# Optimization experiments

Hardware: AMD Instinct MI355X
Metric: run time of the kernel (lower is better)

## Reference

```python
import jax, jax.numpy as jnp
import numpy as np
import math

B, S, D, H, FF = 2, 2048, 1024, 16, 4096
DH = D // H
EPS = 1e-5


def layernorm(x, g, b):
    mu = jnp.mean(x, axis=-1, keepdims=True)
    var = jnp.mean((x - mu) ** 2, axis=-1, keepdims=True)
    return (x - mu) * jax.lax.rsqrt(var + EPS) * g + b


def setup_inputs() -> dict:
    key = jax.random.key(0)
    ks = jax.random.split(key, 8)
    s = lambda fan_in: 1.0 / math.sqrt(fan_in)
    return {
        "x": jax.random.normal(ks[0], (B, S, D), jnp.float32),
        "attention_mask": jnp.zeros((B, 1, 1, S), jnp.float32),
        "wq": jax.random.uniform(ks[1], (D, D), jnp.float32, -s(D), s(D)),
        "wk": jax.random.uniform(ks[2], (D, D), jnp.float32, -s(D), s(D)),
        "wv": jax.random.uniform(ks[3], (D, D), jnp.float32, -s(D), s(D)),
        "wo": jax.random.uniform(ks[4], (D, D), jnp.float32, -s(D), s(D)),
        "w1": jax.random.uniform(ks[5], (D, FF), jnp.float32, -s(D), s(D)),
        "w2": jax.random.uniform(ks[6], (FF, D), jnp.float32, -s(FF), s(FF)),
        "ln1_g": jnp.ones((D,), jnp.float32),
        "ln1_b": jnp.zeros((D,), jnp.float32),
        "ln2_g": jnp.ones((D,), jnp.float32),
        "ln2_b": jnp.zeros((D,), jnp.float32),
    }


def reference(x, attention_mask, wq, wk, wv, wo, w1, w2, ln1_g, ln1_b, ln2_g, ln2_b):
    # --- attention ResNorm (pre-LN) ---
    y = layernorm(x, ln1_g, ln1_b)
    q = (y @ wq).reshape(B, S, H, DH)
    k = (y @ wk).reshape(B, S, H, DH)
    v = (y @ wv).reshape(B, S, H, DH)
    # NOTE: original scales by sqrt(hidden_dim), not sqrt(head_dim)
    scores = jnp.einsum("bqhd,bkhd->bhqk", q, k) / math.sqrt(D) + attention_mask
    probs = jax.nn.softmax(scores, axis=-1)
    attn = jnp.einsum("bhqk,bkhd->bqhd", probs, v).reshape(B, S, D)
    x = x + attn @ wo
    # --- FFN ResNorm ---
    y = layernorm(x, ln2_g, ln2_b)
    y = jax.nn.gelu(y @ w1, approximate=False) @ w2
    return x + y
```

## Files before the change

### kernel.cpp

```cpp
#include <hip/hip_runtime.h>
#include <hip/hip_bf16.h>
#include <math.h>

#define Bb 2
#define Ss 2048
#define Dd 1024
#define Hh 16
#define FFf 4096
#define EPSf 1e-5f
#define SCALEf 0.03125f
#define LOG2Ef 1.4426950408889634f
#define SCALE2f (SCALEf * LOG2Ef)
#define KSPLIT 2
#define NTILES ((Ss / KSPLIT) / 64)

typedef short s16x8 __attribute__((ext_vector_type(8)));
typedef short s16x4 __attribute__((ext_vector_type(4)));
typedef float f32x4 __attribute__((ext_vector_type(4)));
typedef float f32x16 __attribute__((ext_vector_type(16)));

__device__ __forceinline__ short f2bs(float f) {
    union { float f; unsigned u; } v; v.f = f;
    const unsigned r = (v.u + 0x7FFFu + ((v.u >> 16) & 1u)) >> 16;
    return (short)r;
}
__device__ __forceinline__ float bs2f(short s) {
    union { unsigned u; float f; } v; v.u = ((unsigned)(unsigned short)s) << 16;
    return v.f;
}
__device__ __forceinline__ float gelu_exact(float v) {
    return 0.5f * v * (1.0f + erff(v * 0.7071067811865475f));
}
__device__ __forceinline__ void gload16(const void* g, void* l) {
    __builtin_amdgcn_global_load_lds(
        (const __attribute__((address_space(1))) unsigned int*)g,
        (__attribute__((address_space(3))) unsigned int*)l, 16, 0, 0);
}
__device__ __forceinline__ unsigned cvt_pk(float lo, float hi) {
    unsigned r;
    asm("v_cvt_pk_bf16_f32 %0, %1, %2" : "=v"(r) : "v"(lo), "v"(hi));
    return r;
}

__global__ __launch_bounds__(256) void prep(const float* __restrict__ wq, const float* __restrict__ wk,
                                            const float* __restrict__ wv, const float* __restrict__ wo,
                                            const float* __restrict__ w1, const float* __restrict__ w2,
                                            const float* __restrict__ mask,
                                            short* __restrict__ qkvw_t, short* __restrict__ wot,
                                            short* __restrict__ w1t, short* __restrict__ w2t,
                                            float* __restrict__ msc) {
    const int blk = blockIdx.x;
    const int tid = threadIdx.x;
    if (blk >= 3072) {
#pragma unroll
        for (int j = 0; j < 16; ++j) msc[tid + j * 256] = mask[tid + j * 256] * LOG2Ef;
        return;
    }
    const float* W; short* Wt; int K, N, inner;
    if (blk < 1024) {
        const int which = blk >> 8; inner = blk & 255;
        K = 1024; N = 1024;
        W = (which == 0) ? wq : (which == 1) ? wk : (which == 2) ? wv : wo;
        Wt = (which < 3) ? qkvw_t + (size_t)which * 1024 * 1024 : wot;
    } else if (blk < 2048) {
        inner = blk - 1024; K = 1024; N = 4096; W = w1; Wt = w1t;
    } else {
        inner = blk - 2048; K = 4096; N = 1024; W = w2; Wt = w2t;
    }
    const int nbx = N / 64;
    const int bx = inner % nbx, by = inner / nbx;
    __shared__ short T[64][65];
    const int n0 = bx * 64, k0 = by * 64;
    const int c = tid & 63, rg = tid >> 6;
#pragma unroll
    for (int j = 0; j < 16; ++j) {
        const int r = rg * 16 + j;
        T[r][c] = f2bs(W[(size_t)(k0 + r) * N + n0 + c]);
    }
    __syncthreads();
#pragma unroll
    for (int j = 0; j < 16; ++j) {
        const int r = rg * 16 + j;
        Wt[(size_t)(n0 + r) * K + k0 + c] = T[c][r];
    }
}

__global__ __launch_bounds__(256) void vtranspose(const short* __restrict__ QKV,
                                                  short* __restrict__ VT) {
    __shared__ __align__(16) short T[64 * 144];
    const int t = threadIdx.x;
    const int bh = blockIdx.x;
    const int sc = blockIdx.y;
    const int b = bh >> 4, h = bh & 15;
#pragma unroll
    for (int i = 0; i < 4; ++i) {
        const int sl = i * 32 + (t >> 3);
        const int d0 = (t & 7) * 8;
        const s16x8 v = *(const s16x8*)&QKV[((size_t)(b * Ss + sc * 128 + sl)) * 3072 + 2048 + h * 64 + d0];
#pragma unroll
        for (int e = 0; e < 8; ++e) {
            const int d = d0 + e;
            T[(d * 144 + sl) ^ (((d >> 3) & 7) << 3)] = v[e];
        }
    }
    __syncthreads();
#pragma unroll
    for (int i = 0; i < 4; ++i) {
        const int d = i * 16 + (t >> 4);
        const int s0 = (t & 15) * 8;
        const s16x8 o = *(const s16x8*)&T[(d * 144 + s0) ^ (((d >> 3) & 7) << 3)];
        *(s16x8*)&VT[((size_t)(bh * 64 + d)) * 2048 + sc * 128 + s0] = o;
    }
}

__global__ __launch_bounds__(256) void layernorm_bf16(const float* __restrict__ X,
                                                      const float* __restrict__ g,
                                                      const float* __restrict__ bta,
                                                      short* __restrict__ Y) {
    __shared__ float red[8];
    const int row = blockIdx.x;
    const int tid = threadIdx.x;
    const size_t base = (size_t)row * Dd + tid * 4;
    const float4 xv = *(const float4*)&X[base];
    float s  = xv.x + xv.y + xv.z + xv.w;
    float sq = xv.x * xv.x + xv.y * xv.y + xv.z * xv.z + xv.w * xv.w;
#pragma unroll
    for (int o = 32; o >= 1; o >>= 1) {
        s  += __shfl_xor(s, o, 64);
        sq += __shfl_xor(sq, o, 64);
    }
    const int lane = tid & 63, wv = tid >> 6;
    if (lane == 0) { red[wv] = s; red[4 + wv] = sq; }
    __syncthreads();
    const float tot  = red[0] + red[1] + red[2] + red[3];
    const float totq = red[4] + red[5] + red[6] + red[7];
    const float mu  = tot * (1.0f / Dd);
    const float var = totq * (1.0f / Dd) - mu * mu;
    const float inv = 1.0f / sqrtf(var + EPSf);
    const float4 gv = *(const float4*)&g[tid * 4];
    const float4 bv = *(const float4*)&bta[tid * 4];
    s16x4 o;
    o[0] = f2bs((xv.x - mu) * inv * gv.x + bv.x);
    o[1] = f2bs((xv.y - mu) * inv * gv.y + bv.y);
    o[2] = f2bs((xv.z - mu) * inv * gv.z + bv.z);
    o[3] = f2bs((xv.w - mu) * inv * gv.w + bv.w);
    *(s16x4*)&Y[base] = o;
}

template <int EPI>
__global__ __launch_bounds__(256) void gemm_m97(const short* __restrict__ A,
                                                const short* __restrict__ Bt,
                                                void* __restrict__ Cout,
                                                int M, int N, int K, int gx) {
    __shared__ short As[128 * 32];
    __shared__ short Bs[128 * 32];
    const int tid = threadIdx.x;
    const int w = tid >> 6, l = tid & 63;
    const int lr = l & 15, lg = l >> 4;
    const int wr = w >> 1, wc = w & 1;

    const int nwg = gridDim.x;
    const int bid = blockIdx.x;
    const int swz = (bid & 7) * (nwg >> 3) + (bid >> 3);
    const int bx = swz % gx, by = swz / gx;

    const int srow = l >> 2;
    const int skb  = (l & 3) * 8;
    const size_t arow0 = (size_t)(by * 128 + w * 32);
    const size_t brow0 = (size_t)(bx * 128 + w * 32);

    f32x4 acc[4][4] = {};

    for (int k0 = 0; k0 < K; k0 += 32) {
        __syncthreads();
#pragma unroll
        for (int j = 0; j < 2; ++j) {
            gload16(A + (arow0 + j * 16 + srow) * K + k0 + skb,
                    &As[(w * 32 + j * 16) * 32]);
            gload16(Bt + (brow0 + j * 16 + srow) * K + k0 + skb,
                    &Bs[(w * 32 + j * 16) * 32]);
        }
        __syncthreads();
        s16x8 a[4], b[4];
#pragma unroll
        for (int m = 0; m < 4; ++m)
            a[m] = *(const s16x8*)&As[(wr * 64 + m * 16 + lr) * 32 + lg * 8];
#pragma unroll
        for (int n = 0; n < 4; ++n)
            b[n] = *(const s16x8*)&Bs[(wc * 64 + n * 16 + lr) * 32 + lg * 8];
#pragma unroll
        for (int n = 0; n < 4; ++n)
#pragma unroll
            for (int m = 0; m < 4; ++m)
                acc[n][m] = __builtin_amdgcn_mfma_f32_16x16x32_bf16(b[n], a[m], acc[n][m], 0, 0, 0);
    }

    const int row0 = by * 128 + wr * 64;
    const int col0 = bx * 128 + wc * 64;
#pragma unroll
    for (int m = 0; m < 4; ++m) {
        const int row = row0 + m * 16 + lr;
#pragma unroll
        for (int n = 0; n < 4; ++n) {
            const int cb = col0 + n * 16 + lg * 4;
            s16x4 o;
#pragma unroll
            for (int r = 0; r < 4; ++r) {
                float v = acc[n][m][r];
                if (EPI == 1) v = gelu_exact(v);
                o[r] = f2bs(v);
            }
            *(s16x4*)&((short*)Cout)[(size_t)row * N + cb] = o;
        }
    }
}

template <int BM, int BN, int BK, int EPI, int MW>
__global__ __launch_bounds__(256, MW) void gemm_v4(const short* __restrict__ A,
                                                   const short* __restrict__ Bt,
                                                   const float* __restrict__ R,
                                                   void* __restrict__ Cout,
                                                   int M, int N, int K, int gx) {
    constexpr int WM = BM / 2, WN = BN / 2;
    constexpr int MF = WM / 16, NF = WN / 16;
    constexpr int S   = BK / 8;
    constexpr int LPR = BK / 8;
    constexpr int RPI = 64 / LPR;
    constexpr int IPWA = (BM / 4) / RPI;
    constexpr int IPWB = (BN / 4) / RPI;
    __shared__ __align__(16) short As[2][BM * BK];
    __shared__ __align__(16) short Bs[2][BN * BK];

    const int tid = threadIdx.x;
    const int w = tid >> 6, l = tid & 63;
    const int lr = l & 15, lg = l >> 4;
    const int wr = w >> 1, wc = w & 1;

    const int nwg = gridDim.x;
    const int bid = blockIdx.x;
    const int swz = (bid & 7) * (nwg >> 3) + (bid >> 3);
    const int bx = swz % gx, by = swz / gx;

    const int lrow = l / LPR;
    const int sslot = ((l % LPR) ^ (((lrow * BK) >> 6) & (S - 1))) * 8;
    const size_t arow0 = (size_t)(by * BM);
    const size_t brow0 = (size_t)(bx * BN);

    f32x4 acc[NF][MF] = {};

    auto STAGE = [&](int bi, int k0) {
#pragma unroll
        for (int j = 0; j < IPWA; ++j) {
            const int r0 = w * (BM / 4) + j * RPI;
            gload16(A + (arow0 + r0 + lrow) * K + k0 + sslot, &As[bi][r0 * BK]);
        }
#pragma unroll
        for (int j = 0; j < IPWB; ++j) {
            const int r0 = w * (BN / 4) + j * RPI;
            gload16(Bt + (brow0 + r0 + lrow) * K + k0 + sslot, &Bs[bi][r0 * BK]);
        }
    };

    int aidx[BK / 32][MF], bidx[BK / 32][NF];
#pragma unroll
    for (int kk = 0; kk < BK / 32; ++kk) {
#pragma unroll
        for (int m = 0; m < MF; ++m) {
            const int r = wr * WM + m * 16 + lr;
            aidx[kk][m] = r * BK + ((kk * 4 + lg) ^ (((r * BK) >> 6) & (S - 1))) * 8;
        }
#pragma unroll
        for (int n = 0; n < NF; ++n) {
            const int r = wc * WN + n * 16 + lr;
            bidx[kk][n] = r * BK + ((kk * 4 + lg) ^ (((r * BK) >> 6) & (S - 1))) * 8;
        }
    }

    const int NKi = K / BK;
    STAGE(0, 0);

#pragma unroll 2
    for (int ks = 0; ks < NKi; ++ks) {
        const int cur = ks & 1;
        asm volatile("s_waitcnt vmcnt(0)" ::: "memory");
        __builtin_amdgcn_s_barrier();
        if (ks + 1 < NKi) STAGE(cur ^ 1, (ks + 1) * BK);

#pragma unroll
        for (int kk = 0; kk < BK / 32; ++kk) {
            s16x8 a[MF], b[NF];
#pragma unroll
            for (int m = 0; m < MF; ++m) a[m] = *(const s16x8*)&As[cur][aidx[kk][m]];
#pragma unroll
            for (int n = 0; n < NF; ++n) b[n] = *(const s16x8*)&Bs[cur][bidx[kk][n]];
#pragma unroll
            for (int n = 0; n < NF; ++n)
#pragma unroll
                for (int m = 0; m < MF; ++m)
                    acc[n][m] = __builtin_amdgcn_mfma_f32_16x16x32_bf16(b[n], a[m], acc[n][m], 0, 0, 0);
        }
    }

    const int row0 = by * BM + wr * WM;
    const int col0 = bx * BN + wc * WN;
#pragma unroll
    for (int m = 0; m < MF; ++m) {
        const int row = row0 + m * 16 + lr;
#pragma unroll
        for (int n = 0; n < NF; ++n) {
            const int cb = col0 + n * 16 + lg * 4;
            if (EPI == 2) {
                float* C = (float*)Cout;
                const f32x4 r4 = *(const f32x4*)&R[(size_t)row * N + cb];
                f32x4 o;
#pragma unroll
                for (int r = 0; r < 4; ++r) o[r] = acc[n][m][r] + r4[r];
                *(f32x4*)&C[(size_t)row * N + cb] = o;
            } else {
                s16x4 o;
#pragma unroll
                for (int r = 0; r < 4; ++r) {
                    float v = acc[n][m][r];
                    if (EPI == 1) v = gelu_exact(v);
                    o[r] = f2bs(v);
                }
                *(s16x4*)&((short*)Cout)[(size_t)row * N + cb] = o;
            }
        }
    }
}

__global__ __launch_bounds__(256, 4) void attn_split(const short* __restrict__ QKV,
                                                     const short* __restrict__ VT,
                                                     const float* __restrict__ MSC,
                                                     short* __restrict__ Opart,
                                                     float2* __restrict__ ML) {
    __shared__ __align__(16) short Kbuf[2][64 * 64];
    __shared__ __align__(16) short Vbuf[2][64 * 64];

    const int tid = threadIdx.x;
    const int w = tid >> 6, l = tid & 63;
    const int col = l & 31;
    const int hi = l >> 5;

    const int bid0 = blockIdx.x;
    const int bid = (bid0 & 7) * (gridDim.x >> 3) + (bid0 >> 3);
    const int part = bid >> 9;
    const int inner = bid & 511;
    const int qt = inner & 15, h = (inner >> 4) & 15, b = inner >> 8;
    const int q0 = qt * 128 + w * 32;
    const int k_base = part * (Ss / KSPLIT);

    s16x8 qf[4];
    {
        const short* qsrc = QKV + ((size_t)(b * Ss + q0 + col)) * 3072 + h * 64 + hi * 8;
        qf[0] = *(const s16x8*)(qsrc);
        qf[1] = *(const s16x8*)(qsrc + 16);
        qf[2] = *(const s16x8*)(qsrc + 32);
        qf[3] = *(const s16x8*)(qsrc + 48);
    }

    const int sr   = l >> 3;
    const int slot = ((l & 7) ^ (sr & 7)) * 8;
    const short* kg = QKV + (size_t)(b * Ss) * 3072 + 1024 + h * 64 + (size_t)sr * 3072 + slot;
    const short* vg = VT + ((size_t)(b * Hh + h) * 64 + sr) * 2048 + k_base + slot;
    const float* mscb = MSC + (size_t)b * Ss + k_base;

    int kidx[2][4], vidx[2][2][2];
#pragma unroll
    for (int sub = 0; sub < 2; ++sub) {
        const int rk = sub * 32 + col;
#pragma unroll
        for (int dd = 0; dd < 4; ++dd)
            kidx[sub][dd] = rk * 64 + ((2 * dd + hi) ^ (rk & 7)) * 8;
#pragma unroll
        for (int kk = 0; kk < 2; ++kk)
#pragma unroll
            for (int dt = 0; dt < 2; ++dt) {
                const int rv = dt * 32 + col;
                vidx[sub][kk][dt] = rv * 64 + ((sub * 4 + 2 * kk + hi) ^ (rv & 7)) * 8;
            }
    }

    f32x16 o_acc[2] = {};
    float m_used = -1e30f, l_run = 0.0f;

    auto STAGE = [&](int bi, int t) {
#pragma unroll
        for (int j = 0; j < 2; ++j) {
            const int r0 = w * 16 + j * 8;
            gload16(kg + (size_t)(k_base + t * 64 + r0) * 3072, &Kbuf[bi][r0 * 64]);
            gload16(vg + (size_t)r0 * 2048 + t * 64,             &Vbuf[bi][r0 * 64]);
        }
    };

    STAGE(0, 0);

#pragma unroll 2
    for (int i = 0; i < NTILES; ++i) {
        const int cur = i & 1;
        asm volatile("s_waitcnt vmcnt(0)" ::: "memory");
        __builtin_amdgcn_s_barrier();
        if (i + 1 < NTILES) STAGE(cur ^ 1, i + 1);

#pragma unroll
        for (int sub = 0; sub < 2; ++sub) {
            f32x16 sa = {};
#pragma unroll
            for (int dd = 0; dd < 4; ++dd) {
                const s16x8 kf = *(const s16x8*)&Kbuf[cur][kidx[sub][dd]];
                sa = __builtin_amdgcn_mfma_f32_32x32x16_bf16(kf, qf[dd], sa, 0, 0, 0);
            }

#pragma unroll
            for (int c4 = 0; c4 < 4; ++c4) {
                const f32x4 mv = *(const f32x4*)&mscb[i * 64 + sub * 32 + 8 * c4 + 4 * hi];
#pragma unroll
                for (int rr = 0; rr < 4; ++rr) sa[c4 * 4 + rr] = sa[c4 * 4 + rr] * SCALE2f + mv[rr];
            }
            float t8[8], t4[4];
#pragma unroll
            for (int r = 0; r < 8; ++r) t8[r] = fmaxf(sa[2 * r], sa[2 * r + 1]);
#pragma unroll
            for (int r = 0; r < 4; ++r) t4[r] = fmaxf(t8[2 * r], t8[2 * r + 1]);
            float tmax = fmaxf(fmaxf(t4[0], t4[1]), fmaxf(t4[2], t4[3]));
            {
                unsigned a = __float_as_uint(tmax), bq = __float_as_uint(tmax);
                asm volatile("v_permlane32_swap_b32 %0, %1" : "+v"(a), "+v"(bq));
                tmax = fmaxf(tmax, __uint_as_float(hi ? a : bq));
            }
            if (__any(tmax > m_used + 8.0f)) {
                const float nm = fmaxf(m_used, tmax);
                const float corr = __builtin_amdgcn_exp2f(m_used - nm);
                m_used = nm;
                l_run *= corr;
#pragma unroll
                for (int dt = 0; dt < 2; ++dt)
#pragma unroll
                    for (int r = 0; r < 16; ++r) o_acc[dt][r] *= corr;
            }

            unsigned wd[8];
            float s8[8];
#pragma unroll
            for (int m8 = 0; m8 < 8; ++m8) {
                const float p0 = __builtin_amdgcn_exp2f(sa[2 * m8]     - m_used);
                const float p1 = __builtin_amdgcn_exp2f(sa[2 * m8 + 1] - m_used);
                s8[m8] = p0 + p1;
                wd[m8] = cvt_pk(p0, p1);
            }
            float s4[4];
#pragma unroll
            for (int r = 0; r < 4; ++r) s4[r] = s8[2 * r] + s8[2 * r + 1];
            l_run += (s4[0] + s4[1]) + (s4[2] + s4[3]);

            unsigned f00 = wd[0], f02 = wd[2];
            asm volatile("v_permlane32_swap_b32 %0, %1" : "+v"(f00), "+v"(f02));
            unsigned f01 = wd[1], f03 = wd[3];
            asm volatile("v_permlane32_swap_b32 %0, %1" : "+v"(f01), "+v"(f03));
            unsigned f10 = wd[4], f12 = wd[6];
            asm volatile("v_permlane32_swap_b32 %0, %1" : "+v"(f10), "+v"(f12));
            unsigned f11 = wd[5], f13 = wd[7];
            asm volatile("v_permlane32_swap_b32 %0, %1" : "+v"(f11), "+v"(f13));
            union { unsigned u[4]; s16x8 v; } pf0, pf1;
            pf0.u[0] = f00; pf0.u[1] = f01; pf0.u[2] = f02; pf0.u[3] = f03;
            pf1.u[0] = f10; pf1.u[1] = f11; pf1.u[2] = f12; pf1.u[3] = f13;

#pragma unroll
            for (int dt = 0; dt < 2; ++dt) {
                const s16x8 v0 = *(const s16x8*)&Vbuf[cur][vidx[sub][0][dt]];
                const s16x8 v1 = *(const s16x8*)&Vbuf[cur][vidx[sub][1][dt]];
                o_acc[dt] = __builtin_amdgcn_mfma_f32_32x32x16_bf16(v0, pf0.v, o_acc[dt], 0, 0, 0);
                o_acc[dt] = __builtin_amdgcn_mfma_f32_32x32x16_bf16(v1, pf1.v, o_acc[dt], 0, 0, 0);
            }
        }
    }

    float l_tot;
    {
        unsigned a = __float_as_uint(l_run), bq = __float_as_uint(l_run);
        asm volatile("v_permlane32_swap_b32 %0, %1" : "+v"(a), "+v"(bq));
        l_tot = l_run + __uint_as_float(hi ? a : bq);
    }
    const size_t tok = (size_t)(b * Ss + q0 + col);
    if (hi == 0) {
        ML[(size_t)part * (Bb * Ss * Hh) + tok * Hh + h] = make_float2(m_used, l_tot);
    }
    short* obase = Opart + (size_t)part * (Bb * Ss) * Dd + tok * Dd + h * 64;
#pragma unroll
    for (int dt = 0; dt < 2; ++dt) {
#pragma unroll
        for (int c4 = 0; c4 < 4; ++c4) {
            s16x4 ov;
#pragma unroll
            for (int rr = 0; rr < 4; ++rr) ov[rr] = f2bs(o_acc[dt][c4 * 4 + rr]);
            *(s16x4*)&obase[dt * 32 + 8 * c4 + 4 * hi] = ov;
        }
    }
}

__global__ __launch_bounds__(256) void attn_combine(const short* __restrict__ Opart,
                                                    const float2* __restrict__ ML,
                                                    short* __restrict__ Oa) {
    const int tok = blockIdx.x;
    const int t = threadIdx.x;
    const int h = t >> 4;
    const int d = (t & 15) * 4;
    float2 ml[KSPLIT];
    float M = -1e30f;
#pragma unroll
    for (int p = 0; p < KSPLIT; ++p) {
        ml[p] = ML[(size_t)p * (Bb * Ss * Hh) + (size_t)tok * Hh + h];
        M = fmaxf(M, ml[p].x);
    }
    float a[KSPLIT], denom = 0.0f;
#pragma unroll
    for (int p = 0; p < KSPLIT; ++p) {
        a[p] = __builtin_amdgcn_exp2f(ml[p].x - M);
        denom += ml[p].y * a[p];
    }
    const float inv = 1.0f / denom;
    const size_t off = (size_t)tok * Dd + h * 64 + d;
    float acc[4] = {};
#pragma unroll
    for (int p = 0; p < KSPLIT; ++p) {
        const s16x4 o4 = *(const s16x4*)&Opart[(size_t)p * (Bb * Ss) * Dd + off];
#pragma unroll
        for (int r = 0; r < 4; ++r) acc[r] += bs2f(o4[r]) * a[p];
    }
    s16x4 o;
#pragma unroll
    for (int r = 0; r < 4; ++r) o[r] = f2bs(acc[r] * inv);
    *(s16x4*)&Oa[off] = o;
}

extern "C" void kernel_launch(void* const* d_in, const int* in_sizes, int n_in,
                              void* d_out, int out_size, void* d_ws, size_t ws_size,
                              hipStream_t stream) {
    const float* x    = (const float*)d_in[0];
    const float* mask = (const float*)d_in[1];
    const float* wq   = (const float*)d_in[2];
    const float* wk   = (const float*)d_in[3];
    const float* wv   = (const float*)d_in[4];
    const float* wo   = (const float*)d_in[5];
    const float* w1   = (const float*)d_in[6];
    const float* w2   = (const float*)d_in[7];
    const float* ln1g = (const float*)d_in[8];
    const float* ln1b = (const float*)d_in[9];
    const float* ln2g = (const float*)d_in[10];
    const float* ln2b = (const float*)d_in[11];
    float* out = (float*)d_out;

    char* p = (char*)d_ws;
    short* qkvw_t = (short*)p; p += (size_t)3072 * 1024 * 2;
    short* wot    = (short*)p; p += (size_t)1024 * 1024 * 2;
    short* w1t    = (short*)p; p += (size_t)4096 * 1024 * 2;
    short* w2t    = (short*)p; p += (size_t)1024 * 4096 * 2;
    short* y_bf   = (short*)p; p += (size_t)4096 * 1024 * 2;
    short* qkv    = (short*)p; p += (size_t)4096 * 3072 * 2;
    short* attn_b = (short*)p; p += (size_t)4096 * 1024 * 2;
    short* y2_bf  = (short*)p; p += (size_t)4096 * 1024 * 2;
    char*  hregion = p;        p += (size_t)4096 * 4096 * 2;
    float* msc    = (float*)p; p += (size_t)Bb * Ss * 4;

    short*  h_bf   = (short*)hregion;
    short*  o_part = (short*)hregion;
    short*  vt     = y_bf;
    float2* ml     = (float2*)qkvw_t;

    const int M = Bb * Ss;

    prep<<<3073, 256, 0, stream>>>(wq, wk, wv, wo, w1, w2, mask, qkvw_t, wot, w1t, w2t, msc);
    layernorm_bf16<<<M, 256, 0, stream>>>(x, ln1g, ln1b, y_bf);
    gemm_m97<0><<<768, 256, 0, stream>>>(y_bf, qkvw_t, qkv, M, 3072, 1024, 24);
    vtranspose<<<dim3(32, 16), 256, 0, stream>>>(qkv, vt);
    attn_split<<<KSPLIT * 512, 256, 0, stream>>>(qkv, vt, msc, o_part, ml);
    attn_combine<<<M, 256, 0, stream>>>(o_part, ml, attn_b);
    gemm_v4<64, 64, 64, 2, 4><<<1024, 256, 0, stream>>>(attn_b, wot, x, out, M, 1024, 1024, 16);
    layernorm_bf16<<<M, 256, 0, stream>>>(out, ln2g, ln2b, y2_bf);
    gemm_m97<1><<<1024, 256, 0, stream>>>(y2_bf, w1t, h_bf, M, 4096, 1024, 32);
    gemm_v4<64, 64, 64, 2, 4><<<1024, 256, 0, stream>>>(h_bf, w2t, out, out, M, 1024, 4096, 16);
}
```

Before: 269.5 us.

## Replace 128x128 GEMM with double-buffered 256x256 tile kernel; add MFMA priority in attention

Replaces the QKV and FFN-up GEMM kernel with a 512-thread, 256x256-tile version. It double-buffers LDS with an XOR-swizzled layout and prefetches the next K slice during compute, aiming to raise data reuse per load and hide global-load latency. It also wraps the attention MFMA blocks in s_setprio to favour matrix instructions. The larger tile cuts the grid to 192 and 256 workgroups, which may leave CUs underused on a 256-CU part, and the wider accumulators raise register pressure.

```diff
diff --git a/kernel.cpp b/kernel.cpp
--- a/kernel.cpp
+++ b/kernel.cpp
@@ -148,57 +148,83 @@
 }
 
 template <int EPI>
-__global__ __launch_bounds__(256) void gemm_m97(const short* __restrict__ A,
+__global__ __launch_bounds__(512) void gemm_256(const short* __restrict__ A,
                                                 const short* __restrict__ Bt,
                                                 void* __restrict__ Cout,
                                                 int M, int N, int K, int gx) {
-    __shared__ short As[128 * 32];
-    __shared__ short Bs[128 * 32];
+    __shared__ __align__(16) short As[2][256 * 32];
+    __shared__ __align__(16) short Bs[2][256 * 32];
+
     const int tid = threadIdx.x;
     const int w = tid >> 6, l = tid & 63;
     const int lr = l & 15, lg = l >> 4;
-    const int wr = w >> 1, wc = w & 1;
+    const int wr = w >> 2, wc = w & 3;
 
     const int nwg = gridDim.x;
     const int bid = blockIdx.x;
     const int swz = (bid & 7) * (nwg >> 3) + (bid >> 3);
     const int bx = swz % gx, by = swz / gx;
 
-    const int srow = l >> 2;
-    const int skb  = (l & 3) * 8;
-    const size_t arow0 = (size_t)(by * 128 + w * 32);
-    const size_t brow0 = (size_t)(bx * 128 + w * 32);
-
-    f32x4 acc[4][4] = {};
-
-    for (int k0 = 0; k0 < K; k0 += 32) {
-        __syncthreads();
+    const int lrow  = l >> 2;
+    const int sslot = ((l & 3) ^ ((lrow >> 1) & 3)) * 8;
+    const size_t arow0 = (size_t)by * 256;
+    const size_t brow0 = (size_t)bx * 256;
+
+    f32x4 acc[8][4] = {};
+
+    auto STAGE = [&](int bi, int k0) {
 #pragma unroll
         for (int j = 0; j < 2; ++j) {
-            gload16(A + (arow0 + j * 16 + srow) * K + k0 + skb,
-                    &As[(w * 32 + j * 16) * 32]);
-            gload16(Bt + (brow0 + j * 16 + srow) * K + k0 + skb,
-                    &Bs[(w * 32 + j * 16) * 32]);
-        }
-        __syncthreads();
-        s16x8 a[4], b[4];
-#pragma unroll
-        for (int m = 0; m < 4; ++m)
-            a[m] = *(const s16x8*)&As[(wr * 64 + m * 16 + lr) * 32 + lg * 8];
-#pragma unroll
-        for (int n = 0; n < 4; ++n)
-            b[n] = *(const s16x8*)&Bs[(wc * 64 + n * 16 + lr) * 32 + lg * 8];
-#pragma unroll
-        for (int n = 0; n < 4; ++n)
-#pragma unroll
-            for (int m = 0; m < 4; ++m)
-                acc[n][m] = __builtin_amdgcn_mfma_f32_16x16x32_bf16(b[n], a[m], acc[n][m], 0, 0, 0);
-    }
-
-    const int row0 = by * 128 + wr * 64;
-    const int col0 = bx * 128 + wc * 64;
-#pragma unroll
-    for (int m = 0; m < 4; ++m) {
+            const int r0 = w * 32 + j * 16;
+            gload16(A + (arow0 + r0 + lrow) * K + k0 + sslot, &As[bi][r0 * 32]);
+        }
+#pragma unroll
+        for (int j = 0; j < 2; ++j) {
+            const int r0 = w * 32 + j * 16;
+            gload16(Bt + (brow0 + r0 + lrow) * K + k0 + sslot, &Bs[bi][r0 * 32]);
+        }
+    };
+
+    int aidx[8], bidx[4];
+#pragma unroll
+    for (int m = 0; m < 8; ++m) {
+        const int r = wr * 128 + m * 16 + lr;
+        aidx[m] = r * 32 + (lg ^ ((r >> 1) & 3)) * 8;
+    }
+#pragma unroll
+    for (int n = 0; n < 4; ++n) {
+        const int r = wc * 64 + n * 16 + lr;
+        bidx[n] = r * 32 + (lg ^ ((r >> 1) & 3)) * 8;
+    }
+
+    const int NKi = K / 32;
+    STAGE(0, 0);
+
+#pragma unroll 2
+    for (int ks = 0; ks < NKi; ++ks) {
+        const int cur = ks & 1;
+        asm volatile("s_waitcnt vmcnt(0)" ::: "memory");
+        __builtin_amdgcn_s_barrier();
+        if (ks + 1 < NKi) STAGE(cur ^ 1, (ks + 1) * 32);
+
+        s16x8 b0 = *(const s16x8*)&Bs[cur][bidx[0]];
+        s16x8 b1 = *(const s16x8*)&Bs[cur][bidx[1]];
+        s16x8 b2 = *(const s16x8*)&Bs[cur][bidx[2]];
+        s16x8 b3 = *(const s16x8*)&Bs[cur][bidx[3]];
+#pragma unroll
+        for (int m = 0; m < 8; ++m) {
+            const s16x8 am = *(const s16x8*)&As[cur][aidx[m]];
+            acc[m][0] = __builtin_amdgcn_mfma_f32_16x16x32_bf16(b0, am, acc[m][0], 0, 0, 0);
+            acc[m][1] = __builtin_amdgcn_mfma_f32_16x16x32_bf16(b1, am, acc[m][1], 0, 0, 0);
+            acc[m][2] = __builtin_amdgcn_mfma_f32_16x16x32_bf16(b2, am, acc[m][2], 0, 0, 0);
+            acc[m][3] = __builtin_amdgcn_mfma_f32_16x16x32_bf16(b3, am, acc[m][3], 0, 0, 0);
+        }
+    }
+
+    const int row0 = by * 256 + wr * 128;
+    const int col0 = bx * 256 + wc * 64;
+#pragma unroll
+    for (int m = 0; m < 8; ++m) {
         const int row = row0 + m * 16 + lr;
 #pragma unroll
         for (int n = 0; n < 4; ++n) {
@@ -206,7 +232,7 @@
             s16x4 o;
 #pragma unroll
             for (int r = 0; r < 4; ++r) {
-                float v = acc[n][m][r];
+                float v = acc[m][n][r];
                 if (EPI == 1) v = gelu_exact(v);
                 o[r] = f2bs(v);
             }
@@ -406,11 +432,13 @@
 #pragma unroll
         for (int sub = 0; sub < 2; ++sub) {
             f32x16 sa = {};
+            __builtin_amdgcn_s_setprio(1);
 #pragma unroll
             for (int dd = 0; dd < 4; ++dd) {
                 const s16x8 kf = *(const s16x8*)&Kbuf[cur][kidx[sub][dd]];
                 sa = __builtin_amdgcn_mfma_f32_32x32x16_bf16(kf, qf[dd], sa, 0, 0, 0);
             }
+            __builtin_amdgcn_s_setprio(0);
 
 #pragma unroll
             for (int c4 = 0; c4 < 4; ++c4) {
@@ -466,6 +494,7 @@
             pf0.u[0] = f00; pf0.u[1] = f01; pf0.u[2] = f02; pf0.u[3] = f03;
             pf1.u[0] = f10; pf1.u[1] = f11; pf1.u[2] = f12; pf1.u[3] = f13;
 
+            __builtin_amdgcn_s_setprio(1);
 #pragma unroll
             for (int dt = 0; dt < 2; ++dt) {
                 const s16x8 v0 = *(const s16x8*)&Vbuf[cur][vidx[sub][0][dt]];
@@ -473,6 +502,7 @@
                 o_acc[dt] = __builtin_amdgcn_mfma_f32_32x32x16_bf16(v0, pf0.v, o_acc[dt], 0, 0, 0);
                 o_acc[dt] = __builtin_amdgcn_mfma_f32_32x32x16_bf16(v1, pf1.v, o_acc[dt], 0, 0, 0);
             }
+            __builtin_amdgcn_s_setprio(0);
         }
     }
 
@@ -572,12 +602,12 @@
 
     prep<<<3073, 256, 0, stream>>>(wq, wk, wv, wo, w1, w2, mask, qkvw_t, wot, w1t, w2t, msc);
     layernorm_bf16<<<M, 256, 0, stream>>>(x, ln1g, ln1b, y_bf);
-    gemm_m97<0><<<768, 256, 0, stream>>>(y_bf, qkvw_t, qkv, M, 3072, 1024, 24);
+    gemm_256<0><<<192, 512, 0, stream>>>(y_bf, qkvw_t, qkv, M, 3072, 1024, 12);
     vtranspose<<<dim3(32, 16), 256, 0, stream>>>(qkv, vt);
     attn_split<<<KSPLIT * 512, 256, 0, stream>>>(qkv, vt, msc, o_part, ml);
     attn_combine<<<M, 256, 0, stream>>>(o_part, ml, attn_b);
     gemm_v4<64, 64, 64, 2, 4><<<1024, 256, 0, stream>>>(attn_b, wot, x, out, M, 1024, 1024, 16);
     layernorm_bf16<<<M, 256, 0, stream>>>(out, ln2g, ln2b, y2_bf);
-    gemm_m97<1><<<1024, 256, 0, stream>>>(y2_bf, w1t, h_bf, M, 4096, 1024, 32);
+    gemm_256<1><<<256, 512, 0, stream>>>(y2_bf, w1t, h_bf, M, 4096, 1024, 16);
     gemm_v4<64, 64, 64, 2, 4><<<1024, 256, 0, stream>>>(h_bf, w2t, out, out, M, 1024, 4096, 16);
 }
```

Result: no change. 268.3 us (-0.4%).
